# Optimization experiments

Measured on AMD Instinct MI355X. Metric: run time of the kernel, lower is better.

## Reference

```python
import jax, jax.numpy as jnp
import numpy as np

C = 64
NUM_GROUPS = 16  # per Normalize() logic for in_channels=64
EPS = 1e-5

def group_norm(x, gamma, beta):
    b, c, h, w, d = x.shape
    xg = x.reshape(b, NUM_GROUPS, c // NUM_GROUPS, h, w, d)
    mean = xg.mean(axis=(2, 3, 4, 5), keepdims=True)
    var = xg.var(axis=(2, 3, 4, 5), keepdims=True)
    xg = (xg - mean) * jax.lax.rsqrt(var + EPS)
    xn = xg.reshape(b, c, h, w, d)
    return xn * gamma[None, :, None, None, None] + beta[None, :, None, None, None]

def conv1x1(x, w, b):
    # 1x1x1 conv3d == channel mixing: w is [out_c, in_c]
    return jnp.einsum('bchwd,oc->bohwd', x, w) + b[None, :, None, None, None]

def setup_inputs() -> dict:
    key = jax.random.key(0)
    ks = jax.random.split(key, 11)
    s = 1.0 / np.sqrt(C)
    return {
        'x': jax.random.normal(ks[0], (2, C, 16, 16, 16), dtype=jnp.float32),
        'norm_w': jnp.ones((C,), jnp.float32),
        'norm_b': jnp.zeros((C,), jnp.float32),
        'q_w': jax.random.uniform(ks[1], (C, C), jnp.float32, -s, s),
        'q_b': jax.random.uniform(ks[2], (C,), jnp.float32, -s, s),
        'k_w': jax.random.uniform(ks[3], (C, C), jnp.float32, -s, s),
        'k_b': jax.random.uniform(ks[4], (C,), jnp.float32, -s, s),
        'v_w': jax.random.uniform(ks[5], (C, C), jnp.float32, -s, s),
        'v_b': jax.random.uniform(ks[6], (C,), jnp.float32, -s, s),
        'proj_w': jax.random.uniform(ks[7], (C, C), jnp.float32, -s, s),
        'proj_b': jax.random.uniform(ks[8], (C,), jnp.float32, -s, s),
    }

def reference(x, norm_w, norm_b, q_w, q_b, k_w, k_b, v_w, v_b, proj_w, proj_b):
    b, c, h, w, d = x.shape
    n = h * w * d
    hn = group_norm(x, norm_w, norm_b)
    q = conv1x1(hn, q_w, q_b).reshape(b, c, n)   # [b, c, n]
    k = conv1x1(hn, k_w, k_b).reshape(b, c, n)
    v = conv1x1(hn, v_w, v_b).reshape(b, c, n)
    scale = c ** (-0.5)
    scores = jnp.einsum('bcq,bck->bqk', q, k) * scale   # [b, n_q, n_k]
    attn = jax.nn.softmax(scores, axis=2)
    out = jnp.einsum('bck,bqk->bcq', v, attn)            # [b, c, n]
    out = out.reshape(b, c, h, w, d)
    out = conv1x1(out, proj_w, proj_b)
    return x + out
```

## Files before the change

kernel.cpp:

```cpp
#include <hip/hip_runtime.h>
#include <hip/hip_bf16.h>

#define B 2
#define C 64
#define N 4096
#define EPS 1e-5f
#define QSCALE_LOG2E 0.18033688f

using short8 = __attribute__((ext_vector_type(8))) short;
using f32x16 = __attribute__((ext_vector_type(16))) float;

__device__ inline short f2bf(float f) {
  __hip_bfloat16 h = __float2bfloat16(f);
  union { __hip_bfloat16 h; short s; } u; u.h = h; return u.s;
}
__device__ inline float bf2f(short s) {
  union { unsigned u; float f; } u;
  u.u = ((unsigned)(unsigned short)s) << 16;
  return u.f;
}
__device__ inline int packbf(float a, float b) {
  return (int)((unsigned short)f2bf(a) | ((unsigned)(unsigned short)f2bf(b) << 16));
}

__global__ __launch_bounds__(256) void gn_part_kernel(
    const float* __restrict__ x, float2* __restrict__ part) {
  int blk = blockIdx.x;
  int bg = blk >> 4, sl = blk & 15;
  const float4* xv = (const float4*)(x + (size_t)bg * 4 * N) + sl * 256;
  int tid = threadIdx.x;
  float4 v = xv[tid];
  float s = v.x + v.y + v.z + v.w;
  float s2 = v.x * v.x + v.y * v.y + v.z * v.z + v.w * v.w;
  __shared__ float ss[256], ss2[256];
  ss[tid] = s; ss2[tid] = s2;
  __syncthreads();
  for (int st = 128; st > 0; st >>= 1) {
    if (tid < st) { ss[tid] += ss[tid + st]; ss2[tid] += ss2[tid + st]; }
    __syncthreads();
  }
  if (tid == 0) part[blk] = make_float2(ss[0], ss2[0]);
}

__global__ __launch_bounds__(128) void gn_final_kernel(
    const float2* __restrict__ part, const float* __restrict__ gw,
    const float* __restrict__ gb, float* __restrict__ ascale,
    float* __restrict__ bshift) {
  int t = threadIdx.x;
  int c = t & 63, b = t >> 6, g = c >> 2;
  int bg = b * 16 + g;
  float s = 0.f, s2 = 0.f;
#pragma unroll
  for (int sl = 0; sl < 16; ++sl) {
    float2 p = part[bg * 16 + sl];
    s += p.x; s2 += p.y;
  }
  float mean = s * (1.f / 16384.f);
  float var = s2 * (1.f / 16384.f) - mean * mean;
  float inv = rsqrtf(var + EPS);
  float a = inv * gw[c];
  ascale[t] = a;
  bshift[t] = gb[c] - mean * a;
}

__global__ __launch_bounds__(256) void qkv_kernel(
    const float* __restrict__ x, const float* __restrict__ ascale,
    const float* __restrict__ bshift,
    const float* __restrict__ qw, const float* __restrict__ qb,
    const float* __restrict__ kw, const float* __restrict__ kb,
    const float* __restrict__ vw, const float* __restrict__ vb,
    short* __restrict__ q_t, short* __restrict__ k_t, short* __restrict__ v_b) {
  int o0 = blockIdx.y * 8, b = blockIdx.z;
  int pos = blockIdx.x * 256 + threadIdx.x;
  const float* xp = x + (size_t)b * C * N + pos;
  const float* as = ascale + b * C;
  const float* bs = bshift + b * C;

  float sq[8], sk[8], sv[8];
#pragma unroll
  for (int j = 0; j < 8; ++j) { sq[j] = 0.f; sk[j] = 0.f; sv[j] = 0.f; }
#pragma unroll
  for (int c = 0; c < C; ++c) {
    float hv = fmaf(xp[(size_t)c * N], as[c], bs[c]);
#pragma unroll
    for (int j = 0; j < 8; ++j) {
      sq[j] = fmaf(qw[(o0 + j) * C + c], hv, sq[j]);
      sk[j] = fmaf(kw[(o0 + j) * C + c], hv, sk[j]);
      sv[j] = fmaf(vw[(o0 + j) * C + c], hv, sv[j]);
    }
  }
  size_t ti = ((size_t)b * N + pos) * C;
  short8 qv, kv;
#pragma unroll
  for (int j = 0; j < 8; ++j) {
    qv[j] = f2bf((sq[j] + qb[o0 + j]) * QSCALE_LOG2E);
    kv[j] = f2bf(sk[j] + kb[o0 + j]);
  }
  *(short8*)&q_t[ti + o0] = qv;
  *(short8*)&k_t[ti + o0] = kv;
#pragma unroll
  for (int j = 0; j < 8; ++j)
    v_b[((size_t)b * C + o0 + j) * N + pos] = f2bf(sv[j] + vb[o0 + j]);
}

__device__ inline void softpack(f32x16& s, int hi, float& lsum,
                                short8& p0, short8& p1) {
  float ps = 0.f;
#pragma unroll
  for (int i = 0; i < 16; ++i) { s[i] = exp2f(s[i]); ps += s[i]; }
  lsum += ps;
  union U { int i[4]; short8 v; } f0, f1;
  {
    int x0 = packbf(s[0], s[1]), z0 = packbf(s[2], s[3]);
    int y0 = packbf(s[4], s[5]), w0 = packbf(s[6], s[7]);
    int xs = __shfl_xor(x0, 32), zs = __shfl_xor(z0, 32);
    int ys = __shfl_xor(y0, 32), ws2 = __shfl_xor(w0, 32);
    f0.i[0] = hi ? ys : x0; f0.i[1] = hi ? ws2 : z0;
    f0.i[2] = hi ? y0 : xs; f0.i[3] = hi ? w0 : zs;
  }
  {
    int x0 = packbf(s[8], s[9]), z0 = packbf(s[10], s[11]);
    int y0 = packbf(s[12], s[13]), w0 = packbf(s[14], s[15]);
    int xs = __shfl_xor(x0, 32), zs = __shfl_xor(z0, 32);
    int ys = __shfl_xor(y0, 32), ws2 = __shfl_xor(w0, 32);
    f1.i[0] = hi ? ys : x0; f1.i[1] = hi ? ws2 : z0;
    f1.i[2] = hi ? y0 : xs; f1.i[3] = hi ? w0 : zs;
  }
  p0 = f0.v; p1 = f1.v;
}

__global__ __launch_bounds__(256) void attn_kernel(
    const short* __restrict__ q_t, const short* __restrict__ k_t,
    const short* __restrict__ v_b, short* __restrict__ opart,
    float* __restrict__ lpart, int segLen, int kseg) {
  int b = blockIdx.z, s = blockIdx.y;
  int l = threadIdx.x & 63;
  int q0 = blockIdx.x * 256 + (threadIdx.x >> 6) * 64;
  int lo5 = l & 31;
  int hi = l >> 5;

  const short* qp = q_t + (size_t)b * N * C;
  const short* kp = k_t + (size_t)b * N * C;
  const short* vp = v_b + (size_t)b * C * N;

  short8 qf[2][4];
#pragma unroll
  for (int qt = 0; qt < 2; ++qt)
#pragma unroll
    for (int t = 0; t < 4; ++t)
      qf[qt][t] = *(const short8*)&qp[(size_t)(q0 + qt * 32 + lo5) * C + t * 16 + hi * 8];

  f32x16 oacc00, oacc01, oacc10, oacc11;
#pragma unroll
  for (int i = 0; i < 16; ++i) { oacc00[i] = 0.f; oacc01[i] = 0.f; oacc10[i] = 0.f; oacc11[i] = 0.f; }
  float lsum[2] = {0.f, 0.f};

  int kbase = s * segLen;

#define LOAD_KF(DST, K0)                                                     \
  _Pragma("unroll") for (int t = 0; t < 4; ++t)                              \
      DST[t] = *(const short8*)&kp[(size_t)((K0) + lo5) * C + t * 16 + hi * 8];
#define LOAD_VF(DST, K0)                                                     \
  DST[0] = *(const short8*)&vp[(size_t)(lo5) * N + (K0) + hi * 8];           \
  DST[1] = *(const short8*)&vp[(size_t)(32 + lo5) * N + (K0) + hi * 8];      \
  DST[2] = *(const short8*)&vp[(size_t)(lo5) * N + (K0) + 16 + hi * 8];      \
  DST[3] = *(const short8*)&vp[(size_t)(32 + lo5) * N + (K0) + 16 + hi * 8];

#define CHUNK(KF, VF)                                                        \
  {                                                                          \
    f32x16 s0_, s1_;                                                         \
    _Pragma("unroll") for (int i = 0; i < 16; ++i) { s0_[i] = 0.f; s1_[i] = 0.f; } \
    __builtin_amdgcn_s_setprio(1);                                           \
    _Pragma("unroll") for (int t = 0; t < 4; ++t) {                          \
      s0_ = __builtin_amdgcn_mfma_f32_32x32x16_bf16(KF[t], qf[0][t], s0_, 0, 0, 0); \
      s1_ = __builtin_amdgcn_mfma_f32_32x32x16_bf16(KF[t], qf[1][t], s1_, 0, 0, 0); \
    }                                                                        \
    __builtin_amdgcn_s_setprio(0);                                           \
    short8 pf00, pf01, pf10, pf11;                                           \
    softpack(s0_, hi, lsum[0], pf00, pf01);                                  \
    softpack(s1_, hi, lsum[1], pf10, pf11);                                  \
    __builtin_amdgcn_s_setprio(1);                                           \
    oacc00 = __builtin_amdgcn_mfma_f32_32x32x16_bf16(VF[0], pf00, oacc00, 0, 0, 0); \
    oacc01 = __builtin_amdgcn_mfma_f32_32x32x16_bf16(VF[1], pf00, oacc01, 0, 0, 0); \
    oacc10 = __builtin_amdgcn_mfma_f32_32x32x16_bf16(VF[0], pf10, oacc10, 0, 0, 0); \
    oacc11 = __builtin_amdgcn_mfma_f32_32x32x16_bf16(VF[1], pf10, oacc11, 0, 0, 0); \
    oacc00 = __builtin_amdgcn_mfma_f32_32x32x16_bf16(VF[2], pf01, oacc00, 0, 0, 0); \
    oacc01 = __builtin_amdgcn_mfma_f32_32x32x16_bf16(VF[3], pf01, oacc01, 0, 0, 0); \
    oacc10 = __builtin_amdgcn_mfma_f32_32x32x16_bf16(VF[2], pf11, oacc10, 0, 0, 0); \
    oacc11 = __builtin_amdgcn_mfma_f32_32x32x16_bf16(VF[3], pf11, oacc11, 0, 0, 0); \
    __builtin_amdgcn_s_setprio(0);                                           \
  }

  short8 kf0[4], kf1[4], vf0[4], vf1[4];
  LOAD_KF(kf0, kbase)
  LOAD_VF(vf0, kbase)

  for (int kc = 0; kc < segLen; kc += 64) {
    int kA = kbase + kc;
    LOAD_KF(kf1, kA + 32)
    LOAD_VF(vf1, kA + 32)
    CHUNK(kf0, vf0)
    int kN = (kc + 64 < segLen) ? (kA + 64) : kA;
    LOAD_KF(kf0, kN)
    LOAD_VF(vf0, kN)
    CHUNK(kf1, vf1)
  }

#pragma unroll
  for (int qt = 0; qt < 2; ++qt) {
    lsum[qt] += __shfl_xor(lsum[qt], 32);
    int qq = q0 + qt * 32 + lo5;
    short* op = opart + (size_t)(b * kseg + s) * C * N;
#pragma unroll
    for (int r = 0; r < 16; ++r) {
      int c = (r & 3) + 8 * (r >> 2) + 4 * hi;
      float v0 = (qt == 0) ? oacc00[r] : oacc10[r];
      float v1 = (qt == 0) ? oacc01[r] : oacc11[r];
      op[(size_t)c * N + qq] = f2bf(v0);
      op[(size_t)(c + 32) * N + qq] = f2bf(v1);
    }
    if (hi == 0) lpart[(size_t)(b * kseg + s) * N + qq] = lsum[qt];
  }
#undef LOAD_KF
#undef LOAD_VF
#undef CHUNK
}

__global__ __launch_bounds__(256) void merge_kernel(
    const short* __restrict__ opart, const float* __restrict__ lpart,
    short* __restrict__ attnout, int kseg) {
  int idx = blockIdx.x * 256 + threadIdx.x;
  int q4 = (idx & 1023) * 4;
  int c = (idx >> 10) & 63;
  int b = idx >> 16;

  float o[4] = {0.f, 0.f, 0.f, 0.f};
  float L[4] = {0.f, 0.f, 0.f, 0.f};
  for (int s = 0; s < kseg; ++s) {
    float4 lv = *(const float4*)&lpart[(size_t)(b * kseg + s) * N + q4];
    L[0] += lv.x; L[1] += lv.y; L[2] += lv.z; L[3] += lv.w;
    short4 ov = *(const short4*)&opart[((size_t)(b * kseg + s) * C + c) * N + q4];
    o[0] += bf2f(ov.x); o[1] += bf2f(ov.y); o[2] += bf2f(ov.z); o[3] += bf2f(ov.w);
  }
  short4 r;
  r.x = f2bf(o[0] / L[0]); r.y = f2bf(o[1] / L[1]);
  r.z = f2bf(o[2] / L[2]); r.w = f2bf(o[3] / L[3]);
  *(short4*)&attnout[(size_t)(b * C + c) * N + q4] = r;
}

__global__ __launch_bounds__(256) void proj_kernel(
    const short* __restrict__ at, const float* __restrict__ pw,
    const float* __restrict__ pb, const float* __restrict__ x,
    float* __restrict__ out) {
  int o0 = blockIdx.y * 8, b = blockIdx.z;
  int pos = blockIdx.x * 256 + threadIdx.x;
  const short* h = at + (size_t)b * C * N + pos;
  float sum[8];
#pragma unroll
  for (int j = 0; j < 8; ++j) sum[j] = 0.f;
#pragma unroll
  for (int c = 0; c < C; ++c) {
    float hv = bf2f(h[(size_t)c * N]);
#pragma unroll
    for (int j = 0; j < 8; ++j) sum[j] = fmaf(pw[(o0 + j) * C + c], hv, sum[j]);
  }
#pragma unroll
  for (int j = 0; j < 8; ++j) {
    size_t oi = (size_t)(b * C + o0 + j) * N + pos;
    out[oi] = x[oi] + sum[j] + pb[o0 + j];
  }
}

extern "C" void kernel_launch(void* const* d_in, const int* in_sizes, int n_in,
                              void* d_out, int out_size, void* d_ws, size_t ws_size,
                              hipStream_t stream) {
  const float* x      = (const float*)d_in[0];
  const float* norm_w = (const float*)d_in[1];
  const float* norm_b = (const float*)d_in[2];
  const float* q_w    = (const float*)d_in[3];
  const float* q_b    = (const float*)d_in[4];
  const float* k_w    = (const float*)d_in[5];
  const float* k_b    = (const float*)d_in[6];
  const float* v_w    = (const float*)d_in[7];
  const float* v_b    = (const float*)d_in[8];
  const float* proj_w = (const float*)d_in[9];
  const float* proj_b = (const float*)d_in[10];
  float* out = (float*)d_out;

  const size_t BCN = (size_t)B * C * N;

  int kseg = 16;
  auto need = [&](int s) -> size_t {
    return BCN * 2 * 4
         + (2 * B * C + 1024 + (size_t)s * B * N) * 4
         + (size_t)s * BCN * 2;
  };
  while (kseg > 1 && need(kseg) > ws_size) kseg >>= 1;
  int segLen = N / kseg;

  short* q_t     = (short*)d_ws;
  short* k_t     = q_t + BCN;
  short* vbuf    = k_t + BCN;
  short* attnout = vbuf + BCN;
  float* ascale  = (float*)(attnout + BCN);
  float* bshift  = ascale + B * C;
  float2* part   = (float2*)(bshift + B * C);
  float* lpart   = (float*)(part + 512);
  short* opart   = (short*)(lpart + (size_t)kseg * B * N);

  gn_part_kernel<<<512, 256, 0, stream>>>(x, part);
  gn_final_kernel<<<1, 128, 0, stream>>>(part, norm_w, norm_b, ascale, bshift);

  qkv_kernel<<<dim3(N / 256, C / 8, B), 256, 0, stream>>>(
      x, ascale, bshift, q_w, q_b, k_w, k_b, v_w, v_b, q_t, k_t, vbuf);

  attn_kernel<<<dim3(N / 256, kseg, B), 256, 0, stream>>>(
      q_t, k_t, vbuf, opart, lpart, segLen, kseg);

  merge_kernel<<<(int)(BCN / 4 / 256), 256, 0, stream>>>(
      opart, lpart, attnout, kseg);

  proj_kernel<<<dim3(N / 256, C / 8, B), 256, 0, stream>>>(
      attnout, proj_w, proj_b, x, out);
}
```

Measured before the change: 77.09 us.

## Shrink attention per-wave query tile to 32 and drop software pipelining

Each wave now handles 32 queries instead of 64, so K/V fragments loaded from global memory are reused across half as many queries and twice as many blocks are launched. The explicit double-buffered K/V prefetch and the s_setprio hints are removed in favour of a simple per-32-key loop. This lowers register pressure and may raise occupancy, but doubles global K/V traffic per query and loses the manual load/compute overlap.

```diff
diff --git a/kernel.cpp b/kernel.cpp
--- a/kernel.cpp
+++ b/kernel.cpp
@@ -135,7 +135,7 @@
     float* __restrict__ lpart, int segLen, int kseg) {
   int b = blockIdx.z, s = blockIdx.y;
   int l = threadIdx.x & 63;
-  int q0 = blockIdx.x * 256 + (threadIdx.x >> 6) * 64;
+  int q0 = blockIdx.x * 128 + (threadIdx.x >> 6) * 32;
   int lo5 = l & 31;
   int hi = l >> 5;
 
@@ -143,87 +143,55 @@
   const short* kp = k_t + (size_t)b * N * C;
   const short* vp = v_b + (size_t)b * C * N;
 
-  short8 qf[2][4];
-#pragma unroll
-  for (int qt = 0; qt < 2; ++qt)
+  short8 qf[4];
+#pragma unroll
+  for (int t = 0; t < 4; ++t)
+    qf[t] = *(const short8*)&qp[(size_t)(q0 + lo5) * C + t * 16 + hi * 8];
+
+  f32x16 oacc0, oacc1;
+#pragma unroll
+  for (int i = 0; i < 16; ++i) { oacc0[i] = 0.f; oacc1[i] = 0.f; }
+  float lsum = 0.f;
+
+  int kbase = s * segLen;
+  for (int kc = 0; kc < segLen; kc += 32) {
+    int k0 = kbase + kc;
+    short8 kf[4];
 #pragma unroll
     for (int t = 0; t < 4; ++t)
-      qf[qt][t] = *(const short8*)&qp[(size_t)(q0 + qt * 32 + lo5) * C + t * 16 + hi * 8];
-
-  f32x16 oacc00, oacc01, oacc10, oacc11;
-#pragma unroll
-  for (int i = 0; i < 16; ++i) { oacc00[i] = 0.f; oacc01[i] = 0.f; oacc10[i] = 0.f; oacc11[i] = 0.f; }
-  float lsum[2] = {0.f, 0.f};
-
-  int kbase = s * segLen;
-
-#define LOAD_KF(DST, K0)                                                     \
-  _Pragma("unroll") for (int t = 0; t < 4; ++t)                              \
-      DST[t] = *(const short8*)&kp[(size_t)((K0) + lo5) * C + t * 16 + hi * 8];
-#define LOAD_VF(DST, K0)                                                     \
-  DST[0] = *(const short8*)&vp[(size_t)(lo5) * N + (K0) + hi * 8];           \
-  DST[1] = *(const short8*)&vp[(size_t)(32 + lo5) * N + (K0) + hi * 8];      \
-  DST[2] = *(const short8*)&vp[(size_t)(lo5) * N + (K0) + 16 + hi * 8];      \
-  DST[3] = *(const short8*)&vp[(size_t)(32 + lo5) * N + (K0) + 16 + hi * 8];
-
-#define CHUNK(KF, VF)                                                        \
-  {                                                                          \
-    f32x16 s0_, s1_;                                                         \
-    _Pragma("unroll") for (int i = 0; i < 16; ++i) { s0_[i] = 0.f; s1_[i] = 0.f; } \
-    __builtin_amdgcn_s_setprio(1);                                           \
-    _Pragma("unroll") for (int t = 0; t < 4; ++t) {                          \
-      s0_ = __builtin_amdgcn_mfma_f32_32x32x16_bf16(KF[t], qf[0][t], s0_, 0, 0, 0); \
-      s1_ = __builtin_amdgcn_mfma_f32_32x32x16_bf16(KF[t], qf[1][t], s1_, 0, 0, 0); \
-    }                                                                        \
-    __builtin_amdgcn_s_setprio(0);                                           \
-    short8 pf00, pf01, pf10, pf11;                                           \
-    softpack(s0_, hi, lsum[0], pf00, pf01);                                  \
-    softpack(s1_, hi, lsum[1], pf10, pf11);                                  \
-    __builtin_amdgcn_s_setprio(1);                                           \
-    oacc00 = __builtin_amdgcn_mfma_f32_32x32x16_bf16(VF[0], pf00, oacc00, 0, 0, 0); \
-    oacc01 = __builtin_amdgcn_mfma_f32_32x32x16_bf16(VF[1], pf00, oacc01, 0, 0, 0); \
-    oacc10 = __builtin_amdgcn_mfma_f32_32x32x16_bf16(VF[0], pf10, oacc10, 0, 0, 0); \
-    oacc11 = __builtin_amdgcn_mfma_f32_32x32x16_bf16(VF[1], pf10, oacc11, 0, 0, 0); \
-    oacc00 = __builtin_amdgcn_mfma_f32_32x32x16_bf16(VF[2], pf01, oacc00, 0, 0, 0); \
-    oacc01 = __builtin_amdgcn_mfma_f32_32x32x16_bf16(VF[3], pf01, oacc01, 0, 0, 0); \
-    oacc10 = __builtin_amdgcn_mfma_f32_32x32x16_bf16(VF[2], pf11, oacc10, 0, 0, 0); \
-    oacc11 = __builtin_amdgcn_mfma_f32_32x32x16_bf16(VF[3], pf11, oacc11, 0, 0, 0); \
-    __builtin_amdgcn_s_setprio(0);                                           \
-  }
-
-  short8 kf0[4], kf1[4], vf0[4], vf1[4];
-  LOAD_KF(kf0, kbase)
-  LOAD_VF(vf0, kbase)
-
-  for (int kc = 0; kc < segLen; kc += 64) {
-    int kA = kbase + kc;
-    LOAD_KF(kf1, kA + 32)
-    LOAD_VF(vf1, kA + 32)
-    CHUNK(kf0, vf0)
-    int kN = (kc + 64 < segLen) ? (kA + 64) : kA;
-    LOAD_KF(kf0, kN)
-    LOAD_VF(vf0, kN)
-    CHUNK(kf1, vf1)
-  }
-
-#pragma unroll
-  for (int qt = 0; qt < 2; ++qt) {
-    lsum[qt] += __shfl_xor(lsum[qt], 32);
-    int qq = q0 + qt * 32 + lo5;
-    short* op = opart + (size_t)(b * kseg + s) * C * N;
-#pragma unroll
-    for (int r = 0; r < 16; ++r) {
-      int c = (r & 3) + 8 * (r >> 2) + 4 * hi;
-      float v0 = (qt == 0) ? oacc00[r] : oacc10[r];
-      float v1 = (qt == 0) ? oacc01[r] : oacc11[r];
-      op[(size_t)c * N + qq] = f2bf(v0);
-      op[(size_t)(c + 32) * N + qq] = f2bf(v1);
-    }
-    if (hi == 0) lpart[(size_t)(b * kseg + s) * N + qq] = lsum[qt];
-  }
-#undef LOAD_KF
-#undef LOAD_VF
-#undef CHUNK
+      kf[t] = *(const short8*)&kp[(size_t)(k0 + lo5) * C + t * 16 + hi * 8];
+    short8 vf[4];
+    vf[0] = *(const short8*)&vp[(size_t)(lo5) * N + k0 + hi * 8];
+    vf[1] = *(const short8*)&vp[(size_t)(32 + lo5) * N + k0 + hi * 8];
+    vf[2] = *(const short8*)&vp[(size_t)(lo5) * N + k0 + 16 + hi * 8];
+    vf[3] = *(const short8*)&vp[(size_t)(32 + lo5) * N + k0 + 16 + hi * 8];
+
+    f32x16 sacc;
+#pragma unroll
+    for (int i = 0; i < 16; ++i) sacc[i] = 0.f;
+#pragma unroll
+    for (int t = 0; t < 4; ++t)
+      sacc = __builtin_amdgcn_mfma_f32_32x32x16_bf16(kf[t], qf[t], sacc, 0, 0, 0);
+
+    short8 pf0, pf1;
+    softpack(sacc, hi, lsum, pf0, pf1);
+
+    oacc0 = __builtin_amdgcn_mfma_f32_32x32x16_bf16(vf[0], pf0, oacc0, 0, 0, 0);
+    oacc1 = __builtin_amdgcn_mfma_f32_32x32x16_bf16(vf[1], pf0, oacc1, 0, 0, 0);
+    oacc0 = __builtin_amdgcn_mfma_f32_32x32x16_bf16(vf[2], pf1, oacc0, 0, 0, 0);
+    oacc1 = __builtin_amdgcn_mfma_f32_32x32x16_bf16(vf[3], pf1, oacc1, 0, 0, 0);
+  }
+
+  lsum += __shfl_xor(lsum, 32);
+  int qq = q0 + lo5;
+  short* op = opart + (size_t)(b * kseg + s) * C * N;
+#pragma unroll
+  for (int r = 0; r < 16; ++r) {
+    int c = (r & 3) + 8 * (r >> 2) + 4 * hi;
+    op[(size_t)c * N + qq] = f2bf(oacc0[r]);
+    op[(size_t)(c + 32) * N + qq] = f2bf(oacc1[r]);
+  }
+  if (hi == 0) lpart[(size_t)(b * kseg + s) * N + qq] = lsum;
 }
 
 __global__ __launch_bounds__(256) void merge_kernel(
@@ -314,7 +282,7 @@
   qkv_kernel<<<dim3(N / 256, C / 8, B), 256, 0, stream>>>(
       x, ascale, bshift, q_w, q_b, k_w, k_b, v_w, v_b, q_t, k_t, vbuf);
 
-  attn_kernel<<<dim3(N / 256, kseg, B), 256, 0, stream>>>(
+  attn_kernel<<<dim3(N / 128, kseg, B), 256, 0, stream>>>(
       q_t, k_t, vbuf, opart, lpart, segLen, kseg);
 
   merge_kernel<<<(int)(BCN / 4 / 256), 256, 0, stream>>>(
```

After: 93.43 us. 1.21x slower.
